# Kernel tuning notes

Measured on AMD Instinct MI355X. Metric: run time of the kernel, lower is better.

Reference implementation:

```python
import jax, jax.numpy as jnp
import numpy as np


def setup_inputs() -> dict:
    key = jax.random.key(0)
    k1, k2 = jax.random.split(key)
    data1 = jax.random.normal(k1, (2, 4, 4096, 3), dtype=jnp.float32)
    data2 = jax.random.normal(k2, (2, 4, 4096, 3), dtype=jnp.float32)
    return {"data1": data1, "data2": data2, "dim": 0}


def reference(data1, data2, dim):
    # dim == 0 -> swapaxes(0, 0) is identity (default path, dist_type=False)
    if dim > 0:
        data1 = jnp.swapaxes(data1, 0, dim)
        data2 = jnp.swapaxes(data2, 0, dim)
    # pairwise euclidean distances: [B, T, N, M]
    diff = data1[..., :, None, :] - data2[..., None, :, :]
    d2_matrix = jnp.sqrt(jnp.sum(diff * diff, axis=-1))
    # nearest-neighbor distance per point in set1: [B, T, N]
    nn_dist = jnp.min(d2_matrix, axis=-1)
    # func_type == mean: reduce over (-2, -1) -> [B]
    return jnp.mean(nn_dist, axis=(-2, -1))
```

## Files before the change

### kernel.cpp

```cpp
#include <hip/hip_runtime.h>
#include <math.h>

constexpr int kB   = 2;
constexpr int kT   = 4;
constexpr int kBT  = kB * kT;
constexpr int kN   = 4096;
constexpr int kR   = 4;
constexpr int kBLK = 256;
constexpr int kSP1 = kR * kBLK;
constexpr int kS1C = kN / kSP1;
constexpr int kSP2 = 128;
constexpr int kS2C = kN / kSP2;
constexpr int kNG  = kSP2 / 4;


__global__ __launch_bounds__(kBLK, 4) void hd_partial(
    const float* __restrict__ d1, const float* __restrict__ d2,
    float* __restrict__ ws)
{
    const int blk = blockIdx.x;
    const int c2  = blk % kS2C;
    const int t2  = blk / kS2C;
    const int c1  = t2 % kS1C;
    const int bt  = t2 / kS1C;

    const int tid = threadIdx.x;

    __shared__ float4 s2[kSP2 * 3 / 4];
    const float4* __restrict__ g2 =
        (const float4*)(d2 + (size_t)bt * kN * 3 + (size_t)c2 * kSP2 * 3);
    if (tid < kSP2 * 3 / 4) s2[tid] = g2[tid];

    const int p0 = c1 * kSP1 + tid;
    const float* __restrict__ base1 = d1 + (size_t)bt * kN * 3;
    float nx[kR], ny[kR], nz[kR], q1[kR], m[kR];
#pragma unroll
    for (int k = 0; k < kR; ++k) {
        const int p = p0 + k * kBLK;
        const float x = base1[p * 3 + 0];
        const float y = base1[p * 3 + 1];
        const float z = base1[p * 3 + 2];
        nx[k] = -2.0f * x; ny[k] = -2.0f * y; nz[k] = -2.0f * z;
        q1[k] = fmaf(x, x, fmaf(y, y, z * z));
        m[k]  = 3.402823466e38f;
    }
    __syncthreads();

#pragma unroll 8
    for (int g = 0; g < kNG; ++g) {
        const float4 A  = s2[3 * g + 0];
        const float4 Bv = s2[3 * g + 1];
        const float4 Cv = s2[3 * g + 2];
        const float px[4] = {A.x, A.w, Bv.z, Cv.y};
        const float py[4] = {A.y, Bv.x, Bv.w, Cv.z};
        const float pz[4] = {A.z, Bv.y, Cv.x, Cv.w};
        float s[4][kR];
#pragma unroll
        for (int j = 0; j < 4; ++j) {
            const float q2 = fmaf(px[j], px[j], fmaf(py[j], py[j], pz[j] * pz[j]));
#pragma unroll
            for (int k = 0; k < kR; ++k) {
                float t = fmaf(px[j], nx[k], q2);
                t = fmaf(py[j], ny[k], t);
                s[j][k] = fmaf(pz[j], nz[k], t);
            }
        }
#pragma unroll
        for (int k = 0; k < kR; ++k) {
            m[k] = fminf(m[k], fminf(s[0][k], s[1][k]));
            m[k] = fminf(m[k], fminf(s[2][k], s[3][k]));
        }
    }

    float* __restrict__ wrow = ws + ((size_t)c2 * kBT + bt) * kN;
#pragma unroll
    for (int k = 0; k < kR; ++k)
        wrow[p0 + k * kBLK] = fmaxf(m[k] + q1[k], 0.0f);
}

__global__ __launch_bounds__(256) void hd_reduce(
    const float* __restrict__ ws, float* __restrict__ out)
{
    const int bt   = blockIdx.x >> 2;
    const int quad = blockIdx.x & 3;
    const int tid  = threadIdx.x;

    float sum = 0.0f;
#pragma unroll
    for (int i = 0; i < 4; ++i) {
        const int p = quad * 1024 + i * 256 + tid;
        float m = 3.402823466e38f;
#pragma unroll
        for (int c2 = 0; c2 < kS2C; ++c2)
            m = fminf(m, ws[((size_t)c2 * kBT + bt) * kN + p]);
        sum += sqrtf(m);
    }

#pragma unroll
    for (int off = 32; off >= 1; off >>= 1)
        sum += __shfl_down(sum, off, 64);

    __shared__ float ls[4];
    if ((tid & 63) == 0) ls[tid >> 6] = sum;
    __syncthreads();
    if (tid == 0) {
        const float tot = ls[0] + ls[1] + ls[2] + ls[3];
        atomicAdd(&out[bt >> 2], tot * (1.0f / (kT * kN)));
    }
}

extern "C" void kernel_launch(void* const* d_in, const int* in_sizes, int n_in,
                              void* d_out, int out_size, void* d_ws, size_t ws_size,
                              hipStream_t stream) {
    const float* d1 = (const float*)d_in[0];
    const float* d2 = (const float*)d_in[1];
    float* out = (float*)d_out;
    float* ws = (float*)d_ws;

    hipMemsetAsync(d_out, 0, (size_t)kB * sizeof(float), stream);

    hd_partial<<<dim3(kBT * kS1C * kS2C), dim3(kBLK), 0, stream>>>(d1, d2, ws);
    hd_reduce<<<dim3(kBT * 4), dim3(256), 0, stream>>>(ws, out);
}
```

Baseline: 80.21 us.

## Read set-2 points directly from global, fold output zeroing into kernel, vectorize reduce

Removes the shared-memory staging of the set-2 tile and its barrier in the partial kernel; every thread now reads the same float4s from global memory, which become uniform, cache-served loads. Drops the separate memset by having block 0 zero the output, saving one launch. Rewrites the reduce kernel to load float4 rows so each thread handles four points with fewer, wider loads. The output zeroing relies on stream ordering before the reduce kernel's atomics, and the uniform global loads may have higher latency than LDS reads.

Result: no change. 79.38 us (-1.0%).

```diff
diff --git a/kernel.cpp b/kernel.cpp
--- a/kernel.cpp
+++ b/kernel.cpp
@@ -16,7 +16,7 @@
 
 __global__ __launch_bounds__(kBLK, 4) void hd_partial(
     const float* __restrict__ d1, const float* __restrict__ d2,
-    float* __restrict__ ws)
+    float* __restrict__ ws, float* __restrict__ out)
 {
     const int blk = blockIdx.x;
     const int c2  = blk % kS2C;
@@ -26,10 +26,7 @@
 
     const int tid = threadIdx.x;
 
-    __shared__ float4 s2[kSP2 * 3 / 4];
-    const float4* __restrict__ g2 =
-        (const float4*)(d2 + (size_t)bt * kN * 3 + (size_t)c2 * kSP2 * 3);
-    if (tid < kSP2 * 3 / 4) s2[tid] = g2[tid];
+    if (blk == 0 && tid < kB) out[tid] = 0.0f;
 
     const int p0 = c1 * kSP1 + tid;
     const float* __restrict__ base1 = d1 + (size_t)bt * kN * 3;
@@ -44,13 +41,15 @@
         q1[k] = fmaf(x, x, fmaf(y, y, z * z));
         m[k]  = 3.402823466e38f;
     }
-    __syncthreads();
 
-#pragma unroll 8
+    const float4* __restrict__ g2 =
+        (const float4*)(d2 + (size_t)bt * kN * 3 + (size_t)c2 * kSP2 * 3);
+
+#pragma unroll 4
     for (int g = 0; g < kNG; ++g) {
-        const float4 A  = s2[3 * g + 0];
-        const float4 Bv = s2[3 * g + 1];
-        const float4 Cv = s2[3 * g + 2];
+        const float4 A  = g2[3 * g + 0];
+        const float4 Bv = g2[3 * g + 1];
+        const float4 Cv = g2[3 * g + 2];
         const float px[4] = {A.x, A.w, Bv.z, Cv.y};
         const float py[4] = {A.y, Bv.x, Bv.w, Cv.z};
         const float pz[4] = {A.z, Bv.y, Cv.x, Cv.w};
@@ -79,22 +78,24 @@
 }
 
 __global__ __launch_bounds__(256) void hd_reduce(
-    const float* __restrict__ ws, float* __restrict__ out)
+    const float4* __restrict__ ws4, float* __restrict__ out)
 {
     const int bt   = blockIdx.x >> 2;
     const int quad = blockIdx.x & 3;
     const int tid  = threadIdx.x;
 
-    float sum = 0.0f;
-#pragma unroll
-    for (int i = 0; i < 4; ++i) {
-        const int p = quad * 1024 + i * 256 + tid;
-        float m = 3.402823466e38f;
-#pragma unroll
-        for (int c2 = 0; c2 < kS2C; ++c2)
-            m = fminf(m, ws[((size_t)c2 * kBT + bt) * kN + p]);
-        sum += sqrtf(m);
+    const int p4 = quad * 256 + tid;
+    float4 m4 = make_float4(3.402823466e38f, 3.402823466e38f,
+                            3.402823466e38f, 3.402823466e38f);
+#pragma unroll 8
+    for (int c2 = 0; c2 < kS2C; ++c2) {
+        const float4 v = ws4[((size_t)c2 * kBT + bt) * (kN / 4) + p4];
+        m4.x = fminf(m4.x, v.x);
+        m4.y = fminf(m4.y, v.y);
+        m4.z = fminf(m4.z, v.z);
+        m4.w = fminf(m4.w, v.w);
     }
+    float sum = sqrtf(m4.x) + sqrtf(m4.y) + sqrtf(m4.z) + sqrtf(m4.w);
 
 #pragma unroll
     for (int off = 32; off >= 1; off >>= 1)
@@ -117,8 +118,6 @@
     float* out = (float*)d_out;
     float* ws = (float*)d_ws;
 
-    hipMemsetAsync(d_out, 0, (size_t)kB * sizeof(float), stream);
-
-    hd_partial<<<dim3(kBT * kS1C * kS2C), dim3(kBLK), 0, stream>>>(d1, d2, ws);
-    hd_reduce<<<dim3(kBT * 4), dim3(256), 0, stream>>>(ws, out);
+    hd_partial<<<dim3(kBT * kS1C * kS2C), dim3(kBLK), 0, stream>>>(d1, d2, ws, out);
+    hd_reduce<<<dim3(kBT * 4), dim3(256), 0, stream>>>((const float4*)ws, out);
 }
```
